# Kernel optimization log

Hardware: AMD Instinct MI355X
Metric: run time of the kernel (lower is better)

Reference implementation:

```python
import jax, jax.numpy as jnp
import numpy as np

N = 4_000_000
G = 8192


def setup_inputs() -> dict:
    key = jax.random.key(0)
    k1, k2, k3, k4, k5 = jax.random.split(key, 5)
    pred_sid = jax.random.randint(k1, (N, 1), 0, G, dtype=jnp.int32)
    rec_hit_id = jax.random.randint(k2, (N, 1), 0, 2, dtype=jnp.int32)
    rechit_energy = jax.random.uniform(k3, (N, 1), dtype=jnp.float32)
    pred_beta = jax.random.uniform(k4, (N, 1), dtype=jnp.float32)
    pred_corr = jax.random.uniform(k5, (N, 1), dtype=jnp.float32)
    return {
        "pred_sid": pred_sid,
        "rec_hit_id": rec_hit_id,
        "rechit_energy": rechit_energy,
        "pred_beta": pred_beta,
        "pred_corr": pred_corr,
        "num_showers": G,
    }


def _per_kind(mask, sid, energy, beta, corr, num_showers):
    """Per-shower energy sum over `mask` elements and corr factor at the
    max-beta element within the mask (0 if the mask is empty for a shower)."""
    neg_inf = jnp.float32(-jnp.inf)
    e_sum = jax.ops.segment_sum(jnp.where(mask, energy, 0.0), sid,
                                num_segments=num_showers)          # [G]
    beta_m = jnp.where(mask, beta, neg_inf)                         # [N]
    beta_max = jax.ops.segment_max(beta_m, sid, num_segments=num_showers)  # [G]
    is_arg = mask & (beta_m == beta_max[sid])                       # [N]
    corr_g = jax.ops.segment_max(jnp.where(is_arg, corr, neg_inf), sid,
                                 num_segments=num_showers)          # [G]
    has_any = jax.ops.segment_sum(mask.astype(jnp.float32), sid,
                                  num_segments=num_showers) > 0.0   # [G]
    corr_g = jnp.where(has_any, corr_g, 0.0)
    e_corr = corr_g * e_sum                                          # [G]
    return e_sum, e_corr


def reference(pred_sid, rec_hit_id, rechit_energy, pred_beta, pred_corr,
              num_showers):
    sid = pred_sid.reshape(-1)
    is_track = rec_hit_id.reshape(-1).astype(bool)
    energy = rechit_energy.reshape(-1)
    beta = pred_beta.reshape(-1)
    corr = pred_corr.reshape(-1)

    e_raw_hit_g, e_cor_hit_g = _per_kind(~is_track, sid, energy, beta, corr,
                                         num_showers)
    e_raw_trk_g, e_cor_trk_g = _per_kind(is_track, sid, energy, beta, corr,
                                         num_showers)

    # Broadcast per-shower scalars back to every element of the shower
    energy_raw_hits = e_raw_hit_g[sid][:, None]
    energy_corrected_hits = e_cor_hit_g[sid][:, None]
    energy_raw_tracks = e_raw_trk_g[sid][:, None]
    energy_corrected_tracks = e_cor_trk_g[sid][:, None]

    prefer_tracks_raw = jnp.where(energy_raw_tracks != 0, energy_raw_tracks,
                                  energy_raw_hits)
    prefer_tracks_corrected = jnp.where(energy_corrected_tracks != 0,
                                        energy_corrected_tracks,
                                        energy_corrected_hits)
    prefer_hits_raw = jnp.where(energy_raw_hits != 0, energy_raw_hits,
                                energy_raw_tracks)
    prefer_hits_corrected = jnp.where(energy_corrected_hits != 0,
                                      energy_corrected_hits,
                                      energy_corrected_tracks)

    # order: tracks_raw, tracks_corrected, hits_raw, hits_corrected,
    #        prefer_tracks_raw, prefer_tracks_corrected,
    #        prefer_hits_raw, prefer_hits_corrected
    return jnp.stack([
        energy_raw_tracks, energy_corrected_tracks,
        energy_raw_hits, energy_corrected_hits,
        prefer_tracks_raw, prefer_tracks_corrected,
        prefer_hits_raw, prefer_hits_corrected,
    ], axis=0)
```

## Files before the change

kernel.cpp:

```cpp
#include <hip/hip_runtime.h>
#include <stdint.h>

#define G_SHOWERS 8192
#define NBINS (2 * G_SHOWERS)

typedef float f32x4 __attribute__((ext_vector_type(4)));


__global__ __launch_bounds__(1024) void bmax_kernel(
    const int* __restrict__ sid, const int* __restrict__ hitid,
    const float* __restrict__ beta, unsigned* __restrict__ partial,
    unsigned* __restrict__ corr_g, int n) {
    __shared__ unsigned bm[NBINS];
    for (int i = threadIdx.x; i < NBINS; i += 1024) bm[i] = 0u;
    if (blockIdx.x == 0) {
        for (int i = threadIdx.x; i < NBINS; i += 1024) corr_g[i] = 0u;
    }
    __syncthreads();

    const int tid = blockIdx.x * blockDim.x + threadIdx.x;
    const int stride = gridDim.x * blockDim.x;
    const int nv = n >> 2;
    for (int i = tid; i < nv; i += stride) {
        int4   s4 = reinterpret_cast<const int4*>(sid)[i];
        int4   h4 = reinterpret_cast<const int4*>(hitid)[i];
        float4 b4 = reinterpret_cast<const float4*>(beta)[i];
        const int* sp = (const int*)&s4;
        const int* hp = (const int*)&h4;
        const float* bp = (const float*)&b4;
        #pragma unroll
        for (int j = 0; j < 4; ++j) {
            int bin = (hp[j] != 0 ? G_SHOWERS : 0) + sp[j];
            atomicMax(&bm[bin], __float_as_uint(bp[j]));
        }
    }
    for (int i = nv * 4 + tid; i < n; i += stride) {
        int bin = (hitid[i] != 0 ? G_SHOWERS : 0) + sid[i];
        atomicMax(&bm[bin], __float_as_uint(beta[i]));
    }

    __syncthreads();
    unsigned* out = partial + (size_t)blockIdx.x * NBINS;
    for (int i = threadIdx.x; i < NBINS; i += 1024) out[i] = bm[i];
}

__global__ __launch_bounds__(256) void bmax_reduce(
    const unsigned* __restrict__ partial, unsigned* __restrict__ bmax_g, int nb) {
    const int q = threadIdx.x >> 6;
    const int lane = threadIdx.x & 63;
    const int bin = blockIdx.x * 64 + lane;
    unsigned m = 0u;
    #pragma unroll 8
    for (int b = q; b < nb; b += 4)
        m = max(m, partial[(size_t)b * NBINS + bin]);
    __shared__ unsigned red[4][64];
    red[q][lane] = m;
    __syncthreads();
    if (q == 0) {
        m = max(max(red[0][lane], red[1][lane]),
                max(red[2][lane], red[3][lane]));
        bmax_g[bin] = m;
    }
}

__global__ __launch_bounds__(1024) void esum_corr_kernel(
    const int* __restrict__ sid, const int* __restrict__ hitid,
    const float* __restrict__ energy, const float* __restrict__ beta,
    const float* __restrict__ corr, const unsigned* __restrict__ bmax_g,
    float* __restrict__ partial_e, unsigned* __restrict__ corr_g, int n) {
    __shared__ float es[NBINS];
    for (int i = threadIdx.x; i < NBINS; i += 1024) es[i] = 0.0f;
    __syncthreads();

    const int tid = blockIdx.x * blockDim.x + threadIdx.x;
    const int stride = gridDim.x * blockDim.x;
    const int nv = n >> 2;
    for (int i = tid; i < nv; i += stride) {
        int4   s4 = reinterpret_cast<const int4*>(sid)[i];
        int4   h4 = reinterpret_cast<const int4*>(hitid)[i];
        float4 e4 = reinterpret_cast<const float4*>(energy)[i];
        float4 b4 = reinterpret_cast<const float4*>(beta)[i];
        float4 c4 = reinterpret_cast<const float4*>(corr)[i];
        const int* sp = (const int*)&s4;
        const int* hp = (const int*)&h4;
        const float* ep = (const float*)&e4;
        const float* bp = (const float*)&b4;
        const float* cp = (const float*)&c4;
        #pragma unroll
        for (int j = 0; j < 4; ++j) {
            int bin = (hp[j] != 0 ? G_SHOWERS : 0) + sp[j];
            atomicAdd(&es[bin], ep[j]);
            if (__float_as_uint(bp[j]) == __ldg(&bmax_g[bin])) {
                atomicMax(&corr_g[bin], __float_as_uint(cp[j]));
            }
        }
    }
    for (int i = nv * 4 + tid; i < n; i += stride) {
        int bin = (hitid[i] != 0 ? G_SHOWERS : 0) + sid[i];
        atomicAdd(&es[bin], energy[i]);
        if (__float_as_uint(beta[i]) == __ldg(&bmax_g[bin])) {
            atomicMax(&corr_g[bin], __float_as_uint(corr[i]));
        }
    }

    __syncthreads();
    float* out = partial_e + (size_t)blockIdx.x * NBINS;
    for (int i = threadIdx.x; i < NBINS; i += 1024) out[i] = es[i];
}

__global__ __launch_bounds__(256) void table_kernel(
    const float* __restrict__ partial_e, const unsigned* __restrict__ corr_g,
    float* __restrict__ table, int nb) {
    const int q = threadIdx.x >> 6;
    const int lane = threadIdx.x & 63;
    const int g = blockIdx.x * 64 + lane;
    float ah = 0.0f, at = 0.0f;
    #pragma unroll 8
    for (int b = q; b < nb; b += 4) {
        const float* p = partial_e + (size_t)b * NBINS;
        ah += p[g];
        at += p[G_SHOWERS + g];
    }
    __shared__ float rh[4][64], rt[4][64];
    rh[q][lane] = ah;
    rt[q][lane] = at;
    __syncthreads();
    if (q == 0) {
        float raw_hit = rh[0][lane] + rh[1][lane] + rh[2][lane] + rh[3][lane];
        float raw_trk = rt[0][lane] + rt[1][lane] + rt[2][lane] + rt[3][lane];
        float corr_hit = __uint_as_float(corr_g[g]);
        float corr_trk = __uint_as_float(corr_g[G_SHOWERS + g]);
        float cor_hit = corr_hit * raw_hit;
        float cor_trk = corr_trk * raw_trk;

        float4 lo, hi;
        lo.x = raw_trk;
        lo.y = cor_trk;
        lo.z = raw_hit;
        lo.w = cor_hit;
        hi.x = (raw_trk != 0.0f) ? raw_trk : raw_hit;
        hi.y = (cor_trk != 0.0f) ? cor_trk : cor_hit;
        hi.z = (raw_hit != 0.0f) ? raw_hit : raw_trk;
        hi.w = (cor_hit != 0.0f) ? cor_hit : cor_trk;

        reinterpret_cast<float4*>(table)[2 * g]     = lo;
        reinterpret_cast<float4*>(table)[2 * g + 1] = hi;
    }
}

__global__ void gather_kernel(const int* __restrict__ sid,
                              const float* __restrict__ table,
                              float* __restrict__ out, int n) {
    const int tid = blockIdx.x * blockDim.x + threadIdx.x;
    const int stride = gridDim.x * blockDim.x;
    const int nv = n >> 2;
    const float4* tbl = reinterpret_cast<const float4*>(table);

    for (int i = tid; i < nv; i += stride) {
        int4 s4 = reinterpret_cast<const int4*>(sid)[i];

        float4 ax = tbl[2 * s4.x], bx = tbl[2 * s4.x + 1];
        float4 ay = tbl[2 * s4.y], by = tbl[2 * s4.y + 1];
        float4 az = tbl[2 * s4.z], bz = tbl[2 * s4.z + 1];
        float4 aw = tbl[2 * s4.w], bw = tbl[2 * s4.w + 1];

        f32x4 p;
        p.x = ax.x; p.y = ay.x; p.z = az.x; p.w = aw.x;
        __builtin_nontemporal_store(p, reinterpret_cast<f32x4*>(out + 0ll * n) + i);
        p.x = ax.y; p.y = ay.y; p.z = az.y; p.w = aw.y;
        __builtin_nontemporal_store(p, reinterpret_cast<f32x4*>(out + 1ll * n) + i);
        p.x = ax.z; p.y = ay.z; p.z = az.z; p.w = aw.z;
        __builtin_nontemporal_store(p, reinterpret_cast<f32x4*>(out + 2ll * n) + i);
        p.x = ax.w; p.y = ay.w; p.z = az.w; p.w = aw.w;
        __builtin_nontemporal_store(p, reinterpret_cast<f32x4*>(out + 3ll * n) + i);
        p.x = bx.x; p.y = by.x; p.z = bz.x; p.w = bw.x;
        __builtin_nontemporal_store(p, reinterpret_cast<f32x4*>(out + 4ll * n) + i);
        p.x = bx.y; p.y = by.y; p.z = bz.y; p.w = bw.y;
        __builtin_nontemporal_store(p, reinterpret_cast<f32x4*>(out + 5ll * n) + i);
        p.x = bx.z; p.y = by.z; p.z = bz.z; p.w = bw.z;
        __builtin_nontemporal_store(p, reinterpret_cast<f32x4*>(out + 6ll * n) + i);
        p.x = bx.w; p.y = by.w; p.z = bz.w; p.w = bw.w;
        __builtin_nontemporal_store(p, reinterpret_cast<f32x4*>(out + 7ll * n) + i);
    }
    for (int i = nv * 4 + tid; i < n; i += stride) {
        int s = sid[i];
        #pragma unroll
        for (int k = 0; k < 8; ++k) {
            out[(long long)k * n + i] = table[8 * s + k];
        }
    }
}

extern "C" void kernel_launch(void* const* d_in, const int* in_sizes, int n_in,
                              void* d_out, int out_size, void* d_ws, size_t ws_size,
                              hipStream_t stream) {
    const int*   sid    = (const int*)d_in[0];
    const int*   hitid  = (const int*)d_in[1];
    const float* energy = (const float*)d_in[2];
    const float* beta   = (const float*)d_in[3];
    const float* corr   = (const float*)d_in[4];
    const int n = in_sizes[0];

    const size_t slab_bytes = (size_t)NBINS * 4;
    const size_t fixed_bytes = 6 * slab_bytes;
    int nb = 256;
    if (ws_size < (size_t)nb * slab_bytes + fixed_bytes) {
        size_t avail = (ws_size > fixed_bytes) ? (ws_size - fixed_bytes) : slab_bytes;
        nb = (int)(avail / slab_bytes) & ~3;
        if (nb < 8) nb = 8;
    }

    char* base = (char*)d_ws;
    unsigned* partial_b = (unsigned*)base;
    float*    partial_e = (float*)base;
    unsigned* bmax_g    = (unsigned*)(base + (size_t)nb * slab_bytes);
    unsigned* corr_g    = (unsigned*)((char*)bmax_g + slab_bytes);
    float*    table     = (float*)((char*)corr_g + slab_bytes);

    bmax_kernel<<<nb, 1024, 0, stream>>>(sid, hitid, beta, partial_b, corr_g, n);
    bmax_reduce<<<NBINS / 64, 256, 0, stream>>>(partial_b, bmax_g, nb);
    esum_corr_kernel<<<nb, 1024, 0, stream>>>(sid, hitid, energy, beta, corr,
                                              bmax_g, partial_e, corr_g, n);
    table_kernel<<<G_SHOWERS / 64, 256, 0, stream>>>(partial_e, corr_g, table, nb);
    gather_kernel<<<2048, 256, 0, stream>>>(sid, table, (float*)d_out, n);
}
```

Measured before the change: 84.88 us.

## Fuse five stages into one cooperative kernel with grid syncs and cached bin indices

Replaces the five kernel launches with a single cooperative kernel that separates the phases (beta max, max reduce, energy sum/corr, table build, gather) with grid.sync. It also writes a compact 16-bit bin index per element during the first pass, so later passes read 2 bytes instead of re-reading sid and hitid. This is meant to remove launch gaps and part of the input re-read traffic. In exchange, the reduce and table phases now run on only nb blocks instead of many small blocks, and the gather runs at one 1024-thread block per slab. The old multi-kernel path is kept as a fallback if the cooperative launch fails.

```diff
diff --git a/kernel.cpp b/kernel.cpp
--- a/kernel.cpp
+++ b/kernel.cpp
@@ -1,11 +1,228 @@
 #include <hip/hip_runtime.h>
+#include <hip/hip_cooperative_groups.h>
 #include <stdint.h>
+
+namespace cg = cooperative_groups;
 
 #define G_SHOWERS 8192
 #define NBINS (2 * G_SHOWERS)
 
 typedef float f32x4 __attribute__((ext_vector_type(4)));
 
+
+__global__ __launch_bounds__(1024, 1) void fused_kernel(
+    const int* __restrict__ sid, const int* __restrict__ hitid,
+    const float* __restrict__ energy, const float* __restrict__ beta,
+    const float* __restrict__ corr, unsigned* __restrict__ partial,
+    unsigned* __restrict__ bmax_g, unsigned* __restrict__ corr_g,
+    float* __restrict__ table, unsigned short* __restrict__ binbuf,
+    float* __restrict__ out, int n, int nbSlabs) {
+    cg::grid_group grid = cg::this_grid();
+    __shared__ unsigned smem_u[NBINS];
+
+    const int tid = threadIdx.x;
+    const int gtid = blockIdx.x * 1024 + tid;
+    const int gstride = gridDim.x * 1024;
+    const int nv = n >> 2;
+    const int lane = tid & 63;
+    const int q = tid >> 6;
+
+    for (int i = tid; i < NBINS; i += 1024) smem_u[i] = 0u;
+    for (int i = gtid; i < NBINS; i += gstride) corr_g[i] = 0u;
+    __syncthreads();
+
+    for (int i = gtid; i < nv; i += gstride) {
+        int4   s4 = reinterpret_cast<const int4*>(sid)[i];
+        int4   h4 = reinterpret_cast<const int4*>(hitid)[i];
+        float4 b4 = reinterpret_cast<const float4*>(beta)[i];
+        const int* sp = (const int*)&s4;
+        const int* hp = (const int*)&h4;
+        const float* bp = (const float*)&b4;
+        ushort4 bv;
+        unsigned short* bvp = (unsigned short*)&bv;
+        #pragma unroll
+        for (int j = 0; j < 4; ++j) {
+            int bin = (hp[j] != 0 ? G_SHOWERS : 0) + sp[j];
+            bvp[j] = (unsigned short)bin;
+            atomicMax(&smem_u[bin], __float_as_uint(bp[j]));
+        }
+        if (binbuf) reinterpret_cast<ushort4*>(binbuf)[i] = bv;
+    }
+    for (int i = nv * 4 + gtid; i < n; i += gstride) {
+        int bin = (hitid[i] != 0 ? G_SHOWERS : 0) + sid[i];
+        atomicMax(&smem_u[bin], __float_as_uint(beta[i]));
+        if (binbuf) binbuf[i] = (unsigned short)bin;
+    }
+
+    __syncthreads();
+    {
+        unsigned* outp = partial + (size_t)blockIdx.x * NBINS;
+        for (int i = tid; i < NBINS; i += 1024) outp[i] = smem_u[i];
+    }
+    grid.sync();
+
+    {
+        const int ngroups = NBINS / 64;
+        const int iters = (ngroups + gridDim.x - 1) / gridDim.x;
+        for (int it = 0; it < iters; ++it) {
+            int gb = it * gridDim.x + blockIdx.x;
+            bool active = gb < ngroups;
+            int bin = gb * 64 + lane;
+            unsigned m = 0u;
+            if (active) {
+                for (int s = q; s < nbSlabs; s += 16)
+                    m = max(m, partial[(size_t)s * NBINS + bin]);
+            }
+            __syncthreads();
+            smem_u[q * 64 + lane] = m;
+            __syncthreads();
+            if (q == 0 && active) {
+                #pragma unroll
+                for (int j = 1; j < 16; ++j) m = max(m, smem_u[j * 64 + lane]);
+                bmax_g[bin] = m;
+            }
+        }
+    }
+    grid.sync();
+
+    {
+        float* es = (float*)smem_u;
+        for (int i = tid; i < NBINS; i += 1024) es[i] = 0.0f;
+        __syncthreads();
+
+        for (int i = gtid; i < nv; i += gstride) {
+            float4 e4 = reinterpret_cast<const float4*>(energy)[i];
+            float4 b4 = reinterpret_cast<const float4*>(beta)[i];
+            float4 c4 = reinterpret_cast<const float4*>(corr)[i];
+            const float* ep = (const float*)&e4;
+            const float* bp = (const float*)&b4;
+            const float* cp = (const float*)&c4;
+            int bins[4];
+            if (binbuf) {
+                ushort4 bv = reinterpret_cast<const ushort4*>(binbuf)[i];
+                bins[0] = bv.x; bins[1] = bv.y; bins[2] = bv.z; bins[3] = bv.w;
+            } else {
+                int4 s4 = reinterpret_cast<const int4*>(sid)[i];
+                int4 h4 = reinterpret_cast<const int4*>(hitid)[i];
+                const int* sp = (const int*)&s4;
+                const int* hp = (const int*)&h4;
+                #pragma unroll
+                for (int j = 0; j < 4; ++j)
+                    bins[j] = (hp[j] != 0 ? G_SHOWERS : 0) + sp[j];
+            }
+            #pragma unroll
+            for (int j = 0; j < 4; ++j) {
+                atomicAdd(&es[bins[j]], ep[j]);
+                if (__float_as_uint(bp[j]) == bmax_g[bins[j]]) {
+                    atomicMax(&corr_g[bins[j]], __float_as_uint(cp[j]));
+                }
+            }
+        }
+        for (int i = nv * 4 + gtid; i < n; i += gstride) {
+            int bin = (hitid[i] != 0 ? G_SHOWERS : 0) + sid[i];
+            atomicAdd(&es[bin], energy[i]);
+            if (__float_as_uint(beta[i]) == bmax_g[bin]) {
+                atomicMax(&corr_g[bin], __float_as_uint(corr[i]));
+            }
+        }
+
+        __syncthreads();
+        float* outp = (float*)(partial + (size_t)blockIdx.x * NBINS);
+        for (int i = tid; i < NBINS; i += 1024) outp[i] = es[i];
+    }
+    grid.sync();
+
+    {
+        const float* pe = (const float*)partial;
+        float* rh = (float*)smem_u;
+        float* rt = ((float*)smem_u) + 1024;
+        const int ngroups = G_SHOWERS / 64;
+        const int iters = (ngroups + gridDim.x - 1) / gridDim.x;
+        for (int it = 0; it < iters; ++it) {
+            int gb = it * gridDim.x + blockIdx.x;
+            bool active = gb < ngroups;
+            int g = gb * 64 + lane;
+            float ah = 0.0f, at = 0.0f;
+            if (active) {
+                for (int s = q; s < nbSlabs; s += 16) {
+                    const float* p = pe + (size_t)s * NBINS;
+                    ah += p[g];
+                    at += p[G_SHOWERS + g];
+                }
+            }
+            __syncthreads();
+            rh[q * 64 + lane] = ah;
+            rt[q * 64 + lane] = at;
+            __syncthreads();
+            if (q == 0 && active) {
+                #pragma unroll
+                for (int j = 1; j < 16; ++j) {
+                    ah += rh[j * 64 + lane];
+                    at += rt[j * 64 + lane];
+                }
+                float corr_hit = __uint_as_float(corr_g[g]);
+                float corr_trk = __uint_as_float(corr_g[G_SHOWERS + g]);
+                float cor_hit = corr_hit * ah;
+                float cor_trk = corr_trk * at;
+                float4 lo, hi;
+                lo.x = at;
+                lo.y = cor_trk;
+                lo.z = ah;
+                lo.w = cor_hit;
+                hi.x = (at != 0.0f) ? at : ah;
+                hi.y = (cor_trk != 0.0f) ? cor_trk : cor_hit;
+                hi.z = (ah != 0.0f) ? ah : at;
+                hi.w = (cor_hit != 0.0f) ? cor_hit : cor_trk;
+                reinterpret_cast<float4*>(table)[2 * g]     = lo;
+                reinterpret_cast<float4*>(table)[2 * g + 1] = hi;
+            }
+        }
+    }
+    grid.sync();
+
+    {
+        const f32x4* tbl = reinterpret_cast<const f32x4*>(table);
+        for (int i = gtid; i < nv; i += gstride) {
+            int s0, s1, s2, s3;
+            if (binbuf) {
+                ushort4 bv = reinterpret_cast<const ushort4*>(binbuf)[i];
+                s0 = bv.x & (G_SHOWERS - 1); s1 = bv.y & (G_SHOWERS - 1);
+                s2 = bv.z & (G_SHOWERS - 1); s3 = bv.w & (G_SHOWERS - 1);
+            } else {
+                int4 s4 = reinterpret_cast<const int4*>(sid)[i];
+                s0 = s4.x; s1 = s4.y; s2 = s4.z; s3 = s4.w;
+            }
+            f32x4 ax = tbl[2 * s0], bx = tbl[2 * s0 + 1];
+            f32x4 ay = tbl[2 * s1], by = tbl[2 * s1 + 1];
+            f32x4 az = tbl[2 * s2], bz = tbl[2 * s2 + 1];
+            f32x4 aw = tbl[2 * s3], bw = tbl[2 * s3 + 1];
+
+            f32x4 p;
+            p.x = ax.x; p.y = ay.x; p.z = az.x; p.w = aw.x;
+            __builtin_nontemporal_store(p, reinterpret_cast<f32x4*>(out + 0ll * n) + i);
+            p.x = ax.y; p.y = ay.y; p.z = az.y; p.w = aw.y;
+            __builtin_nontemporal_store(p, reinterpret_cast<f32x4*>(out + 1ll * n) + i);
+            p.x = ax.z; p.y = ay.z; p.z = az.z; p.w = aw.z;
+            __builtin_nontemporal_store(p, reinterpret_cast<f32x4*>(out + 2ll * n) + i);
+            p.x = ax.w; p.y = ay.w; p.z = az.w; p.w = aw.w;
+            __builtin_nontemporal_store(p, reinterpret_cast<f32x4*>(out + 3ll * n) + i);
+            p.x = bx.x; p.y = by.x; p.z = bz.x; p.w = bw.x;
+            __builtin_nontemporal_store(p, reinterpret_cast<f32x4*>(out + 4ll * n) + i);
+            p.x = bx.y; p.y = by.y; p.z = bz.y; p.w = bw.y;
+            __builtin_nontemporal_store(p, reinterpret_cast<f32x4*>(out + 5ll * n) + i);
+            p.x = bx.z; p.y = by.z; p.z = bz.z; p.w = bw.z;
+            __builtin_nontemporal_store(p, reinterpret_cast<f32x4*>(out + 6ll * n) + i);
+            p.x = bx.w; p.y = by.w; p.z = bz.w; p.w = bw.w;
+            __builtin_nontemporal_store(p, reinterpret_cast<f32x4*>(out + 7ll * n) + i);
+        }
+        for (int i = nv * 4 + gtid; i < n; i += gstride) {
+            int s = sid[i];
+            #pragma unroll
+            for (int k = 0; k < 8; ++k)
+                out[(long long)k * n + i] = table[8 * s + k];
+        }
+    }
+}
 
 __global__ __launch_bounds__(1024) void bmax_kernel(
     const int* __restrict__ sid, const int* __restrict__ hitid,
@@ -13,54 +230,41 @@
     unsigned* __restrict__ corr_g, int n) {
     __shared__ unsigned bm[NBINS];
     for (int i = threadIdx.x; i < NBINS; i += 1024) bm[i] = 0u;
-    if (blockIdx.x == 0) {
+    if (blockIdx.x == 0)
         for (int i = threadIdx.x; i < NBINS; i += 1024) corr_g[i] = 0u;
-    }
-    __syncthreads();
-
+    __syncthreads();
     const int tid = blockIdx.x * blockDim.x + threadIdx.x;
     const int stride = gridDim.x * blockDim.x;
     const int nv = n >> 2;
     for (int i = tid; i < nv; i += stride) {
-        int4   s4 = reinterpret_cast<const int4*>(sid)[i];
-        int4   h4 = reinterpret_cast<const int4*>(hitid)[i];
+        int4 s4 = reinterpret_cast<const int4*>(sid)[i];
+        int4 h4 = reinterpret_cast<const int4*>(hitid)[i];
         float4 b4 = reinterpret_cast<const float4*>(beta)[i];
         const int* sp = (const int*)&s4;
         const int* hp = (const int*)&h4;
         const float* bp = (const float*)&b4;
         #pragma unroll
-        for (int j = 0; j < 4; ++j) {
-            int bin = (hp[j] != 0 ? G_SHOWERS : 0) + sp[j];
-            atomicMax(&bm[bin], __float_as_uint(bp[j]));
-        }
-    }
-    for (int i = nv * 4 + tid; i < n; i += stride) {
-        int bin = (hitid[i] != 0 ? G_SHOWERS : 0) + sid[i];
-        atomicMax(&bm[bin], __float_as_uint(beta[i]));
-    }
-
-    __syncthreads();
-    unsigned* out = partial + (size_t)blockIdx.x * NBINS;
-    for (int i = threadIdx.x; i < NBINS; i += 1024) out[i] = bm[i];
+        for (int j = 0; j < 4; ++j)
+            atomicMax(&bm[(hp[j] != 0 ? G_SHOWERS : 0) + sp[j]], __float_as_uint(bp[j]));
+    }
+    for (int i = nv * 4 + tid; i < n; i += stride)
+        atomicMax(&bm[(hitid[i] != 0 ? G_SHOWERS : 0) + sid[i]], __float_as_uint(beta[i]));
+    __syncthreads();
+    unsigned* outp = partial + (size_t)blockIdx.x * NBINS;
+    for (int i = threadIdx.x; i < NBINS; i += 1024) outp[i] = bm[i];
 }
 
 __global__ __launch_bounds__(256) void bmax_reduce(
     const unsigned* __restrict__ partial, unsigned* __restrict__ bmax_g, int nb) {
-    const int q = threadIdx.x >> 6;
-    const int lane = threadIdx.x & 63;
+    const int qq = threadIdx.x >> 6, lane = threadIdx.x & 63;
     const int bin = blockIdx.x * 64 + lane;
     unsigned m = 0u;
-    #pragma unroll 8
-    for (int b = q; b < nb; b += 4)
-        m = max(m, partial[(size_t)b * NBINS + bin]);
+    for (int b = qq; b < nb; b += 4) m = max(m, partial[(size_t)b * NBINS + bin]);
     __shared__ unsigned red[4][64];
-    red[q][lane] = m;
-    __syncthreads();
-    if (q == 0) {
-        m = max(max(red[0][lane], red[1][lane]),
-                max(red[2][lane], red[3][lane]));
-        bmax_g[bin] = m;
-    }
+    red[qq][lane] = m;
+    __syncthreads();
+    if (qq == 0)
+        bmax_g[bin] = max(max(red[0][lane], red[1][lane]), max(red[2][lane], red[3][lane]));
 }
 
 __global__ __launch_bounds__(1024) void esum_corr_kernel(
@@ -71,13 +275,12 @@
     __shared__ float es[NBINS];
     for (int i = threadIdx.x; i < NBINS; i += 1024) es[i] = 0.0f;
     __syncthreads();
-
     const int tid = blockIdx.x * blockDim.x + threadIdx.x;
     const int stride = gridDim.x * blockDim.x;
     const int nv = n >> 2;
     for (int i = tid; i < nv; i += stride) {
-        int4   s4 = reinterpret_cast<const int4*>(sid)[i];
-        int4   h4 = reinterpret_cast<const int4*>(hitid)[i];
+        int4 s4 = reinterpret_cast<const int4*>(sid)[i];
+        int4 h4 = reinterpret_cast<const int4*>(hitid)[i];
         float4 e4 = reinterpret_cast<const float4*>(energy)[i];
         float4 b4 = reinterpret_cast<const float4*>(beta)[i];
         float4 c4 = reinterpret_cast<const float4*>(corr)[i];
@@ -90,59 +293,47 @@
         for (int j = 0; j < 4; ++j) {
             int bin = (hp[j] != 0 ? G_SHOWERS : 0) + sp[j];
             atomicAdd(&es[bin], ep[j]);
-            if (__float_as_uint(bp[j]) == __ldg(&bmax_g[bin])) {
+            if (__float_as_uint(bp[j]) == __ldg(&bmax_g[bin]))
                 atomicMax(&corr_g[bin], __float_as_uint(cp[j]));
-            }
         }
     }
     for (int i = nv * 4 + tid; i < n; i += stride) {
         int bin = (hitid[i] != 0 ? G_SHOWERS : 0) + sid[i];
         atomicAdd(&es[bin], energy[i]);
-        if (__float_as_uint(beta[i]) == __ldg(&bmax_g[bin])) {
+        if (__float_as_uint(beta[i]) == __ldg(&bmax_g[bin]))
             atomicMax(&corr_g[bin], __float_as_uint(corr[i]));
-        }
-    }
-
-    __syncthreads();
-    float* out = partial_e + (size_t)blockIdx.x * NBINS;
-    for (int i = threadIdx.x; i < NBINS; i += 1024) out[i] = es[i];
+    }
+    __syncthreads();
+    float* outp = partial_e + (size_t)blockIdx.x * NBINS;
+    for (int i = threadIdx.x; i < NBINS; i += 1024) outp[i] = es[i];
 }
 
 __global__ __launch_bounds__(256) void table_kernel(
     const float* __restrict__ partial_e, const unsigned* __restrict__ corr_g,
     float* __restrict__ table, int nb) {
-    const int q = threadIdx.x >> 6;
-    const int lane = threadIdx.x & 63;
+    const int qq = threadIdx.x >> 6, lane = threadIdx.x & 63;
     const int g = blockIdx.x * 64 + lane;
     float ah = 0.0f, at = 0.0f;
-    #pragma unroll 8
-    for (int b = q; b < nb; b += 4) {
+    for (int b = qq; b < nb; b += 4) {
         const float* p = partial_e + (size_t)b * NBINS;
         ah += p[g];
         at += p[G_SHOWERS + g];
     }
     __shared__ float rh[4][64], rt[4][64];
-    rh[q][lane] = ah;
-    rt[q][lane] = at;
-    __syncthreads();
-    if (q == 0) {
+    rh[qq][lane] = ah;
+    rt[qq][lane] = at;
+    __syncthreads();
+    if (qq == 0) {
         float raw_hit = rh[0][lane] + rh[1][lane] + rh[2][lane] + rh[3][lane];
         float raw_trk = rt[0][lane] + rt[1][lane] + rt[2][lane] + rt[3][lane];
-        float corr_hit = __uint_as_float(corr_g[g]);
-        float corr_trk = __uint_as_float(corr_g[G_SHOWERS + g]);
-        float cor_hit = corr_hit * raw_hit;
-        float cor_trk = corr_trk * raw_trk;
-
+        float cor_hit = __uint_as_float(corr_g[g]) * raw_hit;
+        float cor_trk = __uint_as_float(corr_g[G_SHOWERS + g]) * raw_trk;
         float4 lo, hi;
-        lo.x = raw_trk;
-        lo.y = cor_trk;
-        lo.z = raw_hit;
-        lo.w = cor_hit;
+        lo.x = raw_trk; lo.y = cor_trk; lo.z = raw_hit; lo.w = cor_hit;
         hi.x = (raw_trk != 0.0f) ? raw_trk : raw_hit;
         hi.y = (cor_trk != 0.0f) ? cor_trk : cor_hit;
         hi.z = (raw_hit != 0.0f) ? raw_hit : raw_trk;
         hi.w = (cor_hit != 0.0f) ? cor_hit : cor_trk;
-
         reinterpret_cast<float4*>(table)[2 * g]     = lo;
         reinterpret_cast<float4*>(table)[2 * g + 1] = hi;
     }
@@ -154,16 +345,13 @@
     const int tid = blockIdx.x * blockDim.x + threadIdx.x;
     const int stride = gridDim.x * blockDim.x;
     const int nv = n >> 2;
-    const float4* tbl = reinterpret_cast<const float4*>(table);
-
+    const f32x4* tbl = reinterpret_cast<const f32x4*>(table);
     for (int i = tid; i < nv; i += stride) {
         int4 s4 = reinterpret_cast<const int4*>(sid)[i];
-
-        float4 ax = tbl[2 * s4.x], bx = tbl[2 * s4.x + 1];
-        float4 ay = tbl[2 * s4.y], by = tbl[2 * s4.y + 1];
-        float4 az = tbl[2 * s4.z], bz = tbl[2 * s4.z + 1];
-        float4 aw = tbl[2 * s4.w], bw = tbl[2 * s4.w + 1];
-
+        f32x4 ax = tbl[2 * s4.x], bx = tbl[2 * s4.x + 1];
+        f32x4 ay = tbl[2 * s4.y], by = tbl[2 * s4.y + 1];
+        f32x4 az = tbl[2 * s4.z], bz = tbl[2 * s4.z + 1];
+        f32x4 aw = tbl[2 * s4.w], bw = tbl[2 * s4.w + 1];
         f32x4 p;
         p.x = ax.x; p.y = ay.x; p.z = az.x; p.w = aw.x;
         __builtin_nontemporal_store(p, reinterpret_cast<f32x4*>(out + 0ll * n) + i);
@@ -185,9 +373,8 @@
     for (int i = nv * 4 + tid; i < n; i += stride) {
         int s = sid[i];
         #pragma unroll
-        for (int k = 0; k < 8; ++k) {
+        for (int k = 0; k < 8; ++k)
             out[(long long)k * n + i] = table[8 * s + k];
-        }
     }
 }
 
@@ -199,7 +386,8 @@
     const float* energy = (const float*)d_in[2];
     const float* beta   = (const float*)d_in[3];
     const float* corr   = (const float*)d_in[4];
-    const int n = in_sizes[0];
+    int n = in_sizes[0];
+    float* outp = (float*)d_out;
 
     const size_t slab_bytes = (size_t)NBINS * 4;
     const size_t fixed_bytes = 6 * slab_bytes;
@@ -208,19 +396,34 @@
         size_t avail = (ws_size > fixed_bytes) ? (ws_size - fixed_bytes) : slab_bytes;
         nb = (int)(avail / slab_bytes) & ~3;
         if (nb < 8) nb = 8;
+        if (nb > 256) nb = 256;
     }
 
     char* base = (char*)d_ws;
-    unsigned* partial_b = (unsigned*)base;
-    float*    partial_e = (float*)base;
-    unsigned* bmax_g    = (unsigned*)(base + (size_t)nb * slab_bytes);
-    unsigned* corr_g    = (unsigned*)((char*)bmax_g + slab_bytes);
-    float*    table     = (float*)((char*)corr_g + slab_bytes);
-
-    bmax_kernel<<<nb, 1024, 0, stream>>>(sid, hitid, beta, partial_b, corr_g, n);
-    bmax_reduce<<<NBINS / 64, 256, 0, stream>>>(partial_b, bmax_g, nb);
+    unsigned* partial = (unsigned*)base;
+    unsigned* bmax_g  = (unsigned*)(base + (size_t)nb * slab_bytes);
+    unsigned* corr_g  = (unsigned*)((char*)bmax_g + slab_bytes);
+    float*    table   = (float*)((char*)corr_g + slab_bytes);
+    size_t used = (size_t)nb * slab_bytes + fixed_bytes;
+    size_t bin_bytes = ((size_t)n * 2 + 255) & ~(size_t)255;
+    unsigned short* binbuf = nullptr;
+    if (ws_size >= used + bin_bytes)
+        binbuf = (unsigned short*)(base + used);
+
+    void* args[] = {(void*)&sid, (void*)&hitid, (void*)&energy, (void*)&beta,
+                    (void*)&corr, (void*)&partial, (void*)&bmax_g, (void*)&corr_g,
+                    (void*)&table, (void*)&binbuf, (void*)&outp, (void*)&n,
+                    (void*)&nb};
+    hipError_t err = hipLaunchCooperativeKernel((const void*)fused_kernel,
+                                                dim3(nb), dim3(1024), args, 0,
+                                                stream);
+    if (err == hipSuccess) return;
+    (void)hipGetLastError();
+
+    bmax_kernel<<<nb, 1024, 0, stream>>>(sid, hitid, beta, partial, corr_g, n);
+    bmax_reduce<<<NBINS / 64, 256, 0, stream>>>(partial, bmax_g, nb);
     esum_corr_kernel<<<nb, 1024, 0, stream>>>(sid, hitid, energy, beta, corr,
-                                              bmax_g, partial_e, corr_g, n);
-    table_kernel<<<G_SHOWERS / 64, 256, 0, stream>>>(partial_e, corr_g, table, nb);
-    gather_kernel<<<2048, 256, 0, stream>>>(sid, table, (float*)d_out, n);
-}
+                                              bmax_g, (float*)partial, corr_g, n);
+    table_kernel<<<G_SHOWERS / 64, 256, 0, stream>>>((float*)partial, corr_g, table, nb);
+    gather_kernel<<<2048, 256, 0, stream>>>(sid, table, outp, n);
+}
```

Result: slower. 223.5 us (+163.3%).
